# Kernel tuning notes

Hardware: AMD Instinct MI355X
Metric: run time of the kernel (lower is better)

Reference implementation:

```python
import jax, jax.numpy as jnp
import numpy as np

N_NODES = 50000
N_EDGES = 800000
F_IN = 11
HID = 128
N_ACT = 6


def _gcn_conv(x, W, b, src, dst, n):
    # PyG GCNConv: x' = D^{-1/2}(A+I)D^{-1/2} (x W) + b, with self-loops.
    h = x @ W  # [N, H]
    ones = jnp.ones(src.shape[0], dtype=h.dtype)
    deg = jax.ops.segment_sum(ones, dst, num_segments=n) + 1.0  # +1 self-loop
    dinv = jax.lax.rsqrt(deg)
    enorm = dinv[src] * dinv[dst]  # [E]
    msg = h[src] * enorm[:, None]  # gather + scale
    agg = jax.ops.segment_sum(msg, dst, num_segments=n)
    agg = agg + h * (dinv * dinv)[:, None]  # self-loop contribution (norm = 1/deg)
    return agg + b


def _mlp2(x, W1, b1, W2, b2):
    return jax.nn.relu(x @ W1 + b1) @ W2 + b2


def setup_inputs() -> dict:
    key = jax.random.key(0)
    ks = jax.random.split(key, 16)
    def g(k, shape, scale):
        return jax.random.normal(k, shape, dtype=jnp.float32) * scale
    x = g(ks[0], (N_NODES, F_IN), 1.0)
    edge_index = jax.random.randint(ks[1], (2, N_EDGES), 0, N_NODES, dtype=jnp.int64)
    return {
        "x": x,
        "edge_index": edge_index,
        "W1": g(ks[2], (F_IN, HID), 1.0 / np.sqrt(F_IN)),
        "b1": jnp.zeros((HID,), jnp.float32),
        "W2": g(ks[3], (HID, HID), 1.0 / np.sqrt(HID)),
        "b2": jnp.zeros((HID,), jnp.float32),
        "W3": g(ks[4], (HID, HID), 1.0 / np.sqrt(HID)),
        "b3": jnp.zeros((HID,), jnp.float32),
        "Wv1": g(ks[5], (HID, HID), 1.0 / np.sqrt(HID)),
        "bv1": jnp.zeros((HID,), jnp.float32),
        "Wv2": g(ks[6], (HID, 1), 1.0 / np.sqrt(HID)),
        "bv2": jnp.zeros((1,), jnp.float32),
        "Wa1": g(ks[7], (HID, HID), 1.0 / np.sqrt(HID)),
        "ba1": jnp.zeros((HID,), jnp.float32),
        "Wa2": g(ks[8], (HID, N_ACT), 1.0 / np.sqrt(HID)),
        "ba2": jnp.zeros((N_ACT,), jnp.float32),
    }


def reference(x, edge_index, W1, b1, W2, b2, W3, b3,
              Wv1, bv1, Wv2, bv2, Wa1, ba1, Wa2, ba2):
    src, dst = edge_index[0], edge_index[1]
    n = x.shape[0]
    h = jax.nn.relu(_gcn_conv(x, W1, b1, src, dst, n))
    h = jax.nn.relu(_gcn_conv(h, W2, b2, src, dst, n))
    h = jax.nn.relu(_gcn_conv(h, W3, b3, src, dst, n))
    # global_mean_pool with batch = zeros -> single-graph mean over nodes
    g = jnp.mean(h, axis=0, keepdims=True)  # [1, HID]
    value = _mlp2(g, Wv1, bv1, Wv2, bv2)          # [1, 1]
    advantage = _mlp2(g, Wa1, ba1, Wa2, ba2)      # [1, N_ACT]
    q = value + (advantage - jnp.mean(advantage, axis=-1, keepdims=True))
    return q
```

## Files before the change

kernel.cpp:

```cpp
#include <hip/hip_runtime.h>

#define HID 128
#define F_IN 11
#define FP 16
#define N_ACT 6
#define EPB 2048
#define LMAX 6144
#define CAP 8192

typedef __bf16 bf16;
typedef __bf16 v8bf __attribute__((ext_vector_type(8)));
typedef float f32x4 __attribute__((ext_vector_type(4)));
typedef float v2f __attribute__((ext_vector_type(2)));

__device__ inline float lo16(unsigned u) { return __uint_as_float(u << 16); }
__device__ inline float hi16(unsigned u) { return __uint_as_float(u & 0xffff0000u); }
__device__ inline unsigned pk2(float a, float b) {
  union { bf16 h; unsigned short u; } x, y;
  x.h = (bf16)a; y.h = (bf16)b;
  return ((unsigned)y.u << 16) | x.u;
}
__device__ inline v2f fp8_dec_lo(unsigned v) {
  return __builtin_amdgcn_cvt_pk_f32_fp8(v, false);
}
__device__ inline v2f fp8_dec_hi(unsigned v) {
  return __builtin_amdgcn_cvt_pk_f32_fp8(v, true);
}
__device__ inline unsigned fp8_enc2_lo(float a, float b, unsigned old) {
  return __builtin_amdgcn_cvt_pk_fp8_f32(a, b, old, false);
}
__device__ inline unsigned fp8_enc2_hi(float a, float b, unsigned old) {
  return __builtin_amdgcn_cvt_pk_fp8_f32(a, b, old, true);
}
__device__ inline unsigned char fp8_enc1(float v) {
  return (unsigned char)(__builtin_amdgcn_cvt_pk_fp8_f32(v, v, 0u, false) & 0xffu);
}


__global__ __launch_bounds__(256) void k_init(int* __restrict__ gcur,
                                              float* __restrict__ gsum,
                                              unsigned* __restrict__ xsN,
                                              unsigned* __restrict__ H8aN,
                                              unsigned* __restrict__ H8bN, int nbkt) {
  int t = threadIdx.x;
  if (t < nbkt) gcur[t] = t * CAP;
  if (t < HID) gsum[t] = 0.f;
  if (t < 8) xsN[t] = 0u;
  if (t < 32) { H8aN[t] = 0u; H8bN[t] = 0u; }
}


__global__ __launch_bounds__(256) void k_part(const int* __restrict__ esrc,
                                              const int* __restrict__ edst,
                                              int* __restrict__ gcur,
                                              unsigned* __restrict__ ebuf,
                                              const float* __restrict__ W2,
                                              const float* __restrict__ W3,
                                              bf16* __restrict__ WT2,
                                              bf16* __restrict__ WT3,
                                              int E, int nbkt) {
  __shared__ int hist[256], lofs[256], lcur[256], gbase[256];
  __shared__ unsigned sbuf[EPB];
  int t = threadIdx.x;
  hist[t] = 0;
  if (blockIdx.x < 64) {
    int i = blockIdx.x * 256 + t;
    int nn = i >> 7, k = i & 127;
    WT2[i] = (bf16)W2[k * 128 + nn];
    WT3[i] = (bf16)W3[k * 128 + nn];
  }
  __syncthreads();
  int start = blockIdx.x * EPB, end = min(E, start + EPB);
  unsigned u[8];
#pragma unroll
  for (int i = 0; i < 8; ++i) {
    int e = start + t + i * 256;
    if (e < end) {
      int s = esrc[e], d = edst[e];
      u[i] = ((unsigned)d << 16) | (unsigned)s;
      atomicAdd(&hist[d >> 8], 1);
    }
  }
  __syncthreads();
  int h = hist[t];
  lofs[t] = h;
  __syncthreads();
  for (int off = 1; off < 256; off <<= 1) {
    int x = (t >= off) ? lofs[t - off] : 0;
    __syncthreads();
    lofs[t] += x;
    __syncthreads();
  }
  lcur[t] = lofs[t] - h;
  if (t < nbkt && h) gbase[t] = atomicAdd(&gcur[t], h);
  __syncthreads();
#pragma unroll
  for (int i = 0; i < 8; ++i) {
    int e = start + t + i * 256;
    if (e < end) {
      int b = (int)(u[i] >> 24);
      int p = atomicAdd(&lcur[b], 1);
      sbuf[p] = u[i];
    }
  }
  __syncthreads();
  int m = end - start;
  for (int i = t; i < m; i += 256) {
    unsigned v = sbuf[i];
    int b = (int)(v >> 24);
    int excl = lofs[b] - hist[b];
    ebuf[gbase[b] + (i - excl)] = v;
  }
}

__global__ __launch_bounds__(1024) void k_local(const unsigned* __restrict__ ebuf,
                                                const int* __restrict__ gcur,
                                                int2* __restrict__ rbe,
                                                float* __restrict__ dinv,
                                                unsigned short* __restrict__ cs,
                                                const float* __restrict__ x,
                                                bf16* __restrict__ xs, int n) {
  __shared__ int hist[256], lofs[256], cur[256], realh[256];
  __shared__ float dsh[256];
  __shared__ unsigned sb[LMAX];
  int b = blockIdx.x, t = threadIdx.x;
  int rb = b * CAP, re = gcur[b];
  int m = re - rb;
  int nbase = b << 8;
  bool fit = (m <= LMAX);
  if (t < 256) hist[t] = 0;
  __syncthreads();
  if (fit) {
    for (int i = t; i < m; i += 1024) {
      unsigned u = ebuf[rb + i];
      sb[i] = u;
      atomicAdd(&hist[(int)(u >> 16) - nbase], 1);
    }
  } else {
    for (int i = t; i < m; i += 1024)
      atomicAdd(&hist[(int)(ebuf[rb + i] >> 16) - nbase], 1);
  }
  __syncthreads();
  int h = 0, hp = 0;
  if (t < 256) {
    h = hist[t];
    realh[t] = h;
    hp = (h + 15) & ~15;
    lofs[t] = hp;
  }
  __syncthreads();
  for (int off = 1; off < 256; off <<= 1) {
    int v = (t < 256 && t >= off) ? lofs[t - off] : 0;
    __syncthreads();
    if (t < 256) lofs[t] += v;
    __syncthreads();
  }
  if (t < 256) {
    int pexcl = lofs[t] - hp;
    cur[t] = rb + pexcl;
    float dv = rsqrtf((float)h + 1.0f);
    dsh[t] = dv;
    int g = nbase + t;
    if (g < n) {
      rbe[g] = make_int2(rb + pexcl, rb + pexcl + hp);
      dinv[g] = dv;
    }
  }
  __syncthreads();
  if (fit) {
    for (int i = t; i < m; i += 1024) {
      unsigned u = sb[i];
      int p = atomicAdd(&cur[(int)(u >> 16) - nbase], 1);
      cs[p] = (unsigned short)(u & 0xffffu);
    }
  } else {
    for (int i = t; i < m; i += 1024) {
      unsigned u = ebuf[rb + i];
      int p = atomicAdd(&cur[(int)(u >> 16) - nbase], 1);
      cs[p] = (unsigned short)(u & 0xffffu);
    }
  }
  __syncthreads();
  if (t < 256) {
    int hh = realh[t];
    int hpp = (hh + 15) & ~15;
    int base = cur[t];
    for (int i = hh; i < hpp; ++i) cs[base + (i - hh)] = (unsigned short)n;
  }
  for (int i = t; i < 256 * FP; i += 1024) {
    int node = nbase + (i >> 4), c = i & 15;
    if (node < n)
      xs[(size_t)node * FP + c] =
          (bf16)((c < F_IN) ? x[(size_t)node * F_IN + c] * dsh[i >> 4] : 0.f);
  }
}


__global__ __launch_bounds__(256) void k_layer1(const bf16* __restrict__ xs,
                                                const float* __restrict__ dinv,
                                                const int2* __restrict__ rbe,
                                                const unsigned short* __restrict__ cs,
                                                const float* __restrict__ W1,
                                                const float* __restrict__ b1,
                                                unsigned* __restrict__ H8, int n) {
  __shared__ float Ws[F_IN * HID];
  __shared__ float A1s[64][17];
  int tid = threadIdx.x;
  int n0 = blockIdx.x * 64;
  for (int i = tid; i < F_IN * HID; i += 256) Ws[i] = W1[i];
  int wave = tid >> 6, lane = tid & 63;
  int g8 = lane >> 3, c = lane & 7;
  const unsigned* xs2 = (const unsigned*)xs;
#pragma unroll
  for (int r = 0; r < 2; ++r) {
    int row = wave * 16 + r * 8 + g8;
    int node = n0 + row;
    unsigned sv = 0;
    int j = 0, jend = 0;
    float dd = 0.f;
    if (node < n) {
      sv = xs2[(size_t)node * 8 + c];
      int2 be = rbe[node];
      j = be.x; jend = be.y;
      dd = dinv[node];
    }
    float ax = lo16(sv), ay = hi16(sv);
    for (; j < jend; j += 4) {
#pragma unroll
      for (int k = 0; k < 4; ++k) {
        unsigned v = xs2[(size_t)cs[j + k] * 8 + c];
        ax += lo16(v);
        ay += hi16(v);
      }
    }
    A1s[row][c * 2] = ax * dd;
    A1s[row][c * 2 + 1] = ay * dd;
  }
  __syncthreads();
  int tc = tid & 15, tr = tid >> 4;
  float bb[8];
#pragma unroll
  for (int j = 0; j < 8; ++j) bb[j] = b1[tc * 8 + j];
#pragma unroll
  for (int i = 0; i < 4; ++i) {
    int row = tr * 4 + i;
    int node = n0 + row;
    if (node >= n) continue;
    float acc[8];
#pragma unroll
    for (int j = 0; j < 8; ++j) acc[j] = 0.f;
#pragma unroll
    for (int k = 0; k < F_IN; ++k) {
      float xk = A1s[row][k];
      const float* wr = &Ws[k * HID + tc * 8];
#pragma unroll
      for (int j = 0; j < 8; ++j) acc[j] = fmaf(xk, wr[j], acc[j]);
    }
    float dd = dinv[node];
    float o[8];
#pragma unroll
    for (int j = 0; j < 8; ++j) o[j] = fmaxf(acc[j] + bb[j], 0.f) * dd;
    unsigned w0 = 0, w1 = 0;
    w0 = fp8_enc2_lo(o[0], o[1], w0);
    w0 = fp8_enc2_hi(o[2], o[3], w0);
    w1 = fp8_enc2_lo(o[4], o[5], w1);
    w1 = fp8_enc2_hi(o[6], o[7], w1);
    ((uint2*)H8)[(size_t)node * 16 + tc] = make_uint2(w0, w1);
  }
}



#define LOAD8(p, cv)                                      \
  p##0 = tab[(size_t)(cv.x & 0xffffu) * 32 + c];          \
  p##1 = tab[(size_t)(cv.x >> 16) * 32 + c];              \
  p##2 = tab[(size_t)(cv.y & 0xffffu) * 32 + c];          \
  p##3 = tab[(size_t)(cv.y >> 16) * 32 + c];              \
  p##4 = tab[(size_t)(cv.z & 0xffffu) * 32 + c];          \
  p##5 = tab[(size_t)(cv.z >> 16) * 32 + c];              \
  p##6 = tab[(size_t)(cv.w & 0xffffu) * 32 + c];          \
  p##7 = tab[(size_t)(cv.w >> 16) * 32 + c];

#define CONSUME8(p)                                       \
  acc01 += fp8_dec_lo(p##0); acc23 += fp8_dec_hi(p##0);   \
  acc01 += fp8_dec_lo(p##1); acc23 += fp8_dec_hi(p##1);   \
  acc01 += fp8_dec_lo(p##2); acc23 += fp8_dec_hi(p##2);   \
  acc01 += fp8_dec_lo(p##3); acc23 += fp8_dec_hi(p##3);   \
  acc01 += fp8_dec_lo(p##4); acc23 += fp8_dec_hi(p##4);   \
  acc01 += fp8_dec_lo(p##5); acc23 += fp8_dec_hi(p##5);   \
  acc01 += fp8_dec_lo(p##6); acc23 += fp8_dec_hi(p##6);   \
  acc01 += fp8_dec_lo(p##7); acc23 += fp8_dec_hi(p##7);

template <bool FINAL>
__global__ __launch_bounds__(512) void k_layer(const unsigned* __restrict__ tab,
                                               const float* __restrict__ dinv,
                                               const int2* __restrict__ rbe,
                                               const unsigned short* __restrict__ cs,
                                               const bf16* __restrict__ WT,
                                               const float* __restrict__ b,
                                               unsigned char* __restrict__ H8,
                                               float* __restrict__ gsum, int n) {
  __shared__ bf16 Asm[64 * 128];
  __shared__ float colacc[128];
  int tid = threadIdx.x;
  int n0 = blockIdx.x * 64;
  if (FINAL && tid < 128) colacc[tid] = 0.f;
  int wave = tid >> 6, lane = tid & 63;
  int sub = lane >> 5;
  int c = lane & 31;
#pragma unroll
  for (int r = 0; r < 4; ++r) {
    int row = wave * 8 + r * 2 + sub;
    int node = n0 + row;
    v2f acc01 = (v2f){0.f, 0.f}, acc23 = (v2f){0.f, 0.f};
    float dd = 0.f;
    int j = 0, jend = 0;
    if (node < n) {
      unsigned sv = tab[(size_t)node * 32 + c];
      acc01 = fp8_dec_lo(sv);
      acc23 = fp8_dec_hi(sv);
      int2 be = rbe[node];
      j = be.x; jend = be.y;
      dd = dinv[node];
    }
    if (j < jend) {
      unsigned a0, a1, a2, a3, a4, a5, a6, a7;
      unsigned b0, b1, b2, b3, b4, b5, b6, b7;
      uint4 cv0 = *(const uint4*)(cs + j);
      uint4 cv1 = *(const uint4*)(cs + j + 8);
      LOAD8(a, cv0)
      LOAD8(b, cv1)
      j += 16;
      for (; j < jend; j += 16) {
        uint4 nv0 = *(const uint4*)(cs + j);
        CONSUME8(a)
        LOAD8(a, nv0)
        uint4 nv1 = *(const uint4*)(cs + j + 8);
        CONSUME8(b)
        LOAD8(b, nv1)
      }
      CONSUME8(a)
      CONSUME8(b)
    }
    int kc = c >> 1, half = c & 1;
    uint2 w = make_uint2(pk2(acc01.x * dd, acc01.y * dd),
                         pk2(acc23.x * dd, acc23.y * dd));
    *(uint2*)((char*)Asm + row * 256 + ((kc ^ (row & 7)) << 4) + (half << 3)) = w;
  }
  __syncthreads();
  int l15 = lane & 15, g = lane >> 4;
  int rg = (wave & 3) * 16;
  int cg = (wave >> 2) * 64;
  f32x4 acc[4];
#pragma unroll
  for (int f = 0; f < 4; ++f) acc[f] = (f32x4){0.f, 0.f, 0.f, 0.f};
  int arow = rg + l15;
#pragma unroll
  for (int kk = 0; kk < 4; ++kk) {
    int kc = kk * 4 + g;
    v8bf a = *(const v8bf*)((const char*)Asm + arow * 256 + ((kc ^ (arow & 7)) << 4));
#pragma unroll
    for (int f = 0; f < 4; ++f) {
      int nrow = cg + f * 16 + l15;
      v8bf bfr = *(const v8bf*)(WT + (size_t)nrow * 128 + kc * 8);
      acc[f] = __builtin_amdgcn_mfma_f32_16x16x32_bf16(a, bfr, acc[f], 0, 0, 0);
    }
  }
  int nodebase = n0 + rg + g * 4;
  if (FINAL) {
#pragma unroll
    for (int f = 0; f < 4; ++f) {
      int col = cg + f * 16 + l15;
      float bias = b[col];
      float sf = 0.f;
#pragma unroll
      for (int j = 0; j < 4; ++j) {
        int node = nodebase + j;
        if (node < n) sf += fmaxf(acc[f][j] + bias, 0.f);
      }
      atomicAdd(&colacc[col], sf);
    }
    __syncthreads();
    if (tid < 128) atomicAdd(&gsum[tid], colacc[tid]);
  } else {
    float dv[4];
#pragma unroll
    for (int j = 0; j < 4; ++j)
      dv[j] = (nodebase + j < n) ? dinv[nodebase + j] : 1.f;
#pragma unroll
    for (int f = 0; f < 4; ++f) {
      int col = cg + f * 16 + l15;
      float bias = b[col];
#pragma unroll
      for (int j = 0; j < 4; ++j) {
        int node = nodebase + j;
        if (node < n) {
          float v = fmaxf(acc[f][j] + bias, 0.f) * dv[j];
          H8[(size_t)node * 128 + col] = fp8_enc1(v);
        }
      }
    }
  }
}

#undef LOAD8
#undef CONSUME8


__global__ __launch_bounds__(128) void k_head(const float* __restrict__ gsum,
    const float* __restrict__ Wv1, const float* __restrict__ bv1,
    const float* __restrict__ Wv2, const float* __restrict__ bv2,
    const float* __restrict__ Wa1, const float* __restrict__ ba1,
    const float* __restrict__ Wa2, const float* __restrict__ ba2,
    float* __restrict__ out, int n) {
  __shared__ float gs[HID], ha[HID], red[2], advs[N_ACT], vsh;
  int t = threadIdx.x;
  gs[t] = gsum[t] * (1.0f / (float)n);
  __syncthreads();
  float av = bv1[t], aa = ba1[t];
  for (int k = 0; k < HID; ++k) {
    float gk = gs[k];
    av = fmaf(gk, Wv1[k * HID + t], av);
    aa = fmaf(gk, Wa1[k * HID + t], aa);
  }
  float hv = fmaxf(av, 0.f);
  ha[t] = fmaxf(aa, 0.f);
  float pv = hv * Wv2[t];
#pragma unroll
  for (int o = 32; o > 0; o >>= 1) pv += __shfl_down(pv, o);
  if ((t & 63) == 0) red[t >> 6] = pv;
  __syncthreads();
  if (t == 0) vsh = red[0] + red[1] + bv2[0];
  if (t < N_ACT) {
    float adv = ba2[t];
    for (int j = 0; j < HID; ++j) adv = fmaf(ha[j], Wa2[j * N_ACT + t], adv);
    advs[t] = adv;
  }
  __syncthreads();
  if (t < N_ACT) {
    float m = 0.f;
#pragma unroll
    for (int a = 0; a < N_ACT; ++a) m += advs[a];
    m *= (1.0f / N_ACT);
    out[t] = vsh + advs[t] - m;
  }
}


extern "C" void kernel_launch(void* const* d_in, const int* in_sizes, int n_in,
                              void* d_out, int out_size, void* d_ws, size_t ws_size,
                              hipStream_t stream) {
  const float* x   = (const float*)d_in[0];
  const int*   ei  = (const int*)d_in[1];
  const float* W1  = (const float*)d_in[2];
  const float* b1  = (const float*)d_in[3];
  const float* W2  = (const float*)d_in[4];
  const float* b2  = (const float*)d_in[5];
  const float* W3  = (const float*)d_in[6];
  const float* b3  = (const float*)d_in[7];
  const float* Wv1 = (const float*)d_in[8];
  const float* bv1 = (const float*)d_in[9];
  const float* Wv2 = (const float*)d_in[10];
  const float* bv2 = (const float*)d_in[11];
  const float* Wa1 = (const float*)d_in[12];
  const float* ba1 = (const float*)d_in[13];
  const float* Wa2 = (const float*)d_in[14];
  const float* ba2 = (const float*)d_in[15];
  float* out = (float*)d_out;

  const int N = in_sizes[0] / F_IN;
  const int E = in_sizes[1] / 2;
  const int* esrc = ei;
  const int* edst = ei + E;
  const int nbkt = (N + 255) >> 8;
  const int gE = (E + EPB - 1) / EPB;

  char* p = (char*)d_ws;
  auto alloc = [&](size_t bytes) {
    void* r = (void*)p;
    p += (bytes + 1023) & ~(size_t)1023;
    return r;
  };
  unsigned* ebuf   = (unsigned*)alloc((size_t)nbkt * CAP * 4);
  int*   gcur      = (int*)alloc((size_t)nbkt * 4);
  int2*  rbe       = (int2*)alloc((size_t)N * 8);
  float* dinv      = (float*)alloc((size_t)N * 4);
  unsigned short* cs = (unsigned short*)alloc((size_t)nbkt * CAP * 2);
  bf16*  xs        = (bf16*)alloc((size_t)(N + 1) * FP * 2);
  bf16*  WT2       = (bf16*)alloc(128 * 128 * 2);
  bf16*  WT3       = (bf16*)alloc(128 * 128 * 2);
  unsigned* H8a    = (unsigned*)alloc((size_t)(N + 1) * 128);
  unsigned* H8b    = (unsigned*)alloc((size_t)(N + 1) * 128);
  float* gsum      = (float*)alloc(HID * 4);

  k_init<<<1, 256, 0, stream>>>(gcur, gsum, (unsigned*)(xs + (size_t)N * FP),
                                H8a + (size_t)N * 32, H8b + (size_t)N * 32, nbkt);
  k_part<<<gE, 256, 0, stream>>>(esrc, edst, gcur, ebuf, W2, W3, WT2, WT3, E, nbkt);
  k_local<<<nbkt, 1024, 0, stream>>>(ebuf, gcur, rbe, dinv, cs, x, xs, N);

  k_layer1<<<(N + 63) / 64, 256, 0, stream>>>(xs, dinv, rbe, cs, W1, b1, H8a, N);

  int gL = (N + 63) / 64;
  k_layer<false><<<gL, 512, 0, stream>>>(H8a, dinv, rbe, cs, WT2, b2,
                                         (unsigned char*)H8b, gsum, N);
  k_layer<true><<<gL, 512, 0, stream>>>(H8b, dinv, rbe, cs, WT3, b3,
                                        (unsigned char*)nullptr, gsum, N);

  k_head<<<1, 128, 0, stream>>>(gsum, Wv1, bv1, Wv2, bv2, Wa1, ba1, Wa2, ba2, out, N);
}
```

Baseline: 147.5 us.

## Gather 4 neighbors per wave with 8-byte loads and shuffle-reduce rows

The aggregation loop in k_layer changes from half-waves each owning a row and reading 4-byte fp8 chunks to a whole wave per row. Each 16-lane quarter handles a different neighbor and reads 8-byte chunks, then partial sums are combined with cross-lane xor shuffles. Neighbor list padding drops from 16 to 8, which cuts padded dummy gathers for the low-degree nodes. The trade-off is fewer loads in flight per lane, the added shuffle reduction cost, and column indices now read as scalar ushort loads rather than vectorized uint4.

Result: slower. 154.2 us (+4.5%).

```diff
diff --git a/kernel.cpp b/kernel.cpp
--- a/kernel.cpp
+++ b/kernel.cpp
@@ -145,7 +145,7 @@
   if (t < 256) {
     h = hist[t];
     realh[t] = h;
-    hp = (h + 15) & ~15;
+    hp = (h + 7) & ~7;
     lofs[t] = hp;
   }
   __syncthreads();
@@ -183,7 +183,7 @@
   __syncthreads();
   if (t < 256) {
     int hh = realh[t];
-    int hpp = (hh + 15) & ~15;
+    int hpp = (hh + 7) & ~7;
     int base = cur[t];
     for (int i = hh; i < hpp; ++i) cs[base + (i - hh)] = (unsigned short)n;
   }
@@ -271,25 +271,9 @@
 
 
 
-#define LOAD8(p, cv)                                      \
-  p##0 = tab[(size_t)(cv.x & 0xffffu) * 32 + c];          \
-  p##1 = tab[(size_t)(cv.x >> 16) * 32 + c];              \
-  p##2 = tab[(size_t)(cv.y & 0xffffu) * 32 + c];          \
-  p##3 = tab[(size_t)(cv.y >> 16) * 32 + c];              \
-  p##4 = tab[(size_t)(cv.z & 0xffffu) * 32 + c];          \
-  p##5 = tab[(size_t)(cv.z >> 16) * 32 + c];              \
-  p##6 = tab[(size_t)(cv.w & 0xffffu) * 32 + c];          \
-  p##7 = tab[(size_t)(cv.w >> 16) * 32 + c];
-
-#define CONSUME8(p)                                       \
-  acc01 += fp8_dec_lo(p##0); acc23 += fp8_dec_hi(p##0);   \
-  acc01 += fp8_dec_lo(p##1); acc23 += fp8_dec_hi(p##1);   \
-  acc01 += fp8_dec_lo(p##2); acc23 += fp8_dec_hi(p##2);   \
-  acc01 += fp8_dec_lo(p##3); acc23 += fp8_dec_hi(p##3);   \
-  acc01 += fp8_dec_lo(p##4); acc23 += fp8_dec_hi(p##4);   \
-  acc01 += fp8_dec_lo(p##5); acc23 += fp8_dec_hi(p##5);   \
-  acc01 += fp8_dec_lo(p##6); acc23 += fp8_dec_hi(p##6);   \
-  acc01 += fp8_dec_lo(p##7); acc23 += fp8_dec_hi(p##7);
+#define DECACC(v)                                   \
+  c0 += fp8_dec_lo(v.x); c1 += fp8_dec_hi(v.x);     \
+  c2 += fp8_dec_lo(v.y); c3 += fp8_dec_hi(v.y);
 
 template <bool FINAL>
 __global__ __launch_bounds__(512) void k_layer(const unsigned* __restrict__ tab,
@@ -306,46 +290,53 @@
   int n0 = blockIdx.x * 64;
   if (FINAL && tid < 128) colacc[tid] = 0.f;
   int wave = tid >> 6, lane = tid & 63;
-  int sub = lane >> 5;
-  int c = lane & 31;
-#pragma unroll
-  for (int r = 0; r < 4; ++r) {
-    int row = wave * 8 + r * 2 + sub;
+  int q = lane & 15;
+  int g4 = lane >> 4;
+  const uint2* tab2 = (const uint2*)tab;
+#pragma unroll 2
+  for (int r = 0; r < 8; ++r) {
+    int row = wave * 8 + r;
     int node = n0 + row;
-    v2f acc01 = (v2f){0.f, 0.f}, acc23 = (v2f){0.f, 0.f};
+    v2f c0 = (v2f){0.f, 0.f}, c1 = (v2f){0.f, 0.f};
+    v2f c2 = (v2f){0.f, 0.f}, c3 = (v2f){0.f, 0.f};
     float dd = 0.f;
+    uint2 sv = make_uint2(0u, 0u);
     int j = 0, jend = 0;
     if (node < n) {
-      unsigned sv = tab[(size_t)node * 32 + c];
-      acc01 = fp8_dec_lo(sv);
-      acc23 = fp8_dec_hi(sv);
+      sv = tab2[(size_t)node * 16 + q];
       int2 be = rbe[node];
       j = be.x; jend = be.y;
       dd = dinv[node];
     }
     if (j < jend) {
-      unsigned a0, a1, a2, a3, a4, a5, a6, a7;
-      unsigned b0, b1, b2, b3, b4, b5, b6, b7;
-      uint4 cv0 = *(const uint4*)(cs + j);
-      uint4 cv1 = *(const uint4*)(cs + j + 8);
-      LOAD8(a, cv0)
-      LOAD8(b, cv1)
-      j += 16;
-      for (; j < jend; j += 16) {
-        uint4 nv0 = *(const uint4*)(cs + j);
-        CONSUME8(a)
-        LOAD8(a, nv0)
-        uint4 nv1 = *(const uint4*)(cs + j + 8);
-        CONSUME8(b)
-        LOAD8(b, nv1)
+      uint2 va = tab2[(size_t)cs[j + g4] * 16 + q];
+      uint2 vb = tab2[(size_t)cs[j + 4 + g4] * 16 + q];
+      j += 8;
+      for (; j < jend; j += 8) {
+        uint2 na = tab2[(size_t)cs[j + g4] * 16 + q];
+        DECACC(va)
+        va = na;
+        uint2 nb = tab2[(size_t)cs[j + 4 + g4] * 16 + q];
+        DECACC(vb)
+        vb = nb;
       }
-      CONSUME8(a)
-      CONSUME8(b)
-    }
-    int kc = c >> 1, half = c & 1;
-    uint2 w = make_uint2(pk2(acc01.x * dd, acc01.y * dd),
-                         pk2(acc23.x * dd, acc23.y * dd));
-    *(uint2*)((char*)Asm + row * 256 + ((kc ^ (row & 7)) << 4) + (half << 3)) = w;
+      DECACC(va)
+      DECACC(vb)
+    }
+    c0.x += __shfl_xor(c0.x, 16); c0.x += __shfl_xor(c0.x, 32);
+    c0.y += __shfl_xor(c0.y, 16); c0.y += __shfl_xor(c0.y, 32);
+    c1.x += __shfl_xor(c1.x, 16); c1.x += __shfl_xor(c1.x, 32);
+    c1.y += __shfl_xor(c1.y, 16); c1.y += __shfl_xor(c1.y, 32);
+    c2.x += __shfl_xor(c2.x, 16); c2.x += __shfl_xor(c2.x, 32);
+    c2.y += __shfl_xor(c2.y, 16); c2.y += __shfl_xor(c2.y, 32);
+    c3.x += __shfl_xor(c3.x, 16); c3.x += __shfl_xor(c3.x, 32);
+    c3.y += __shfl_xor(c3.y, 16); c3.y += __shfl_xor(c3.y, 32);
+    DECACC(sv)
+    if (g4 == 0) {
+      uint4 w = make_uint4(pk2(c0.x * dd, c0.y * dd), pk2(c1.x * dd, c1.y * dd),
+                           pk2(c2.x * dd, c2.y * dd), pk2(c3.x * dd, c3.y * dd));
+      *(uint4*)((char*)Asm + row * 256 + ((q ^ (row & 7)) << 4)) = w;
+    }
   }
   __syncthreads();
   int l15 = lane & 15, g = lane >> 4;
@@ -403,8 +394,7 @@
   }
 }
 
-#undef LOAD8
-#undef CONSUME8
+#undef DECACC
 
 
 __global__ __launch_bounds__(128) void k_head(const float* __restrict__ gsum,
```
